# Performance work log

Hardware: AMD Instinct MI355X
Metric: run time of the kernel (lower is better)

Reference implementation:

```python
import jax, jax.numpy as jnp
import numpy as np

N_NODES = 100000
N_USERS = 60000
N_MOVIES = 40000
N_EDGES = 1200000
D_IN = 64
D_EMB = 64


def setup_inputs() -> dict:
    key = jax.random.key(0)
    ks = jax.random.split(key, 6)
    x = jax.random.normal(ks[0], (N_NODES, D_IN), dtype=jnp.float32)
    edge_index = jax.random.randint(ks[1], (2, N_EDGES), 0, N_NODES, dtype=jnp.int64)
    # Glorot-ish init for the two GCNConv linear weights
    W1 = jax.random.normal(ks[2], (D_IN, D_EMB), dtype=jnp.float32) * (1.0 / np.sqrt(D_IN))
    b1 = jnp.zeros((D_EMB,), dtype=jnp.float32)
    W2 = jax.random.normal(ks[3], (D_EMB, D_EMB), dtype=jnp.float32) * (1.0 / np.sqrt(D_EMB))
    b2 = jnp.zeros((D_EMB,), dtype=jnp.float32)
    return {"x": x, "edge_index": edge_index, "W1": W1, "b1": b1, "W2": W2, "b2": b2}


def gcn_conv(x, W, b, src, dst):
    """PyG GCNConv: D^{-1/2}(A+I)D^{-1/2} X W + b with symmetric norm and self-loops."""
    h = x @ W  # [N, D_out]
    ones = jnp.ones(src.shape[0], dtype=h.dtype)
    # degree includes self-loop (+1)
    deg = jax.ops.segment_sum(ones, dst, num_segments=N_NODES) + 1.0
    dinv = jax.lax.rsqrt(deg)  # [N]
    coef = dinv[src] * dinv[dst]  # [E]
    agg = jax.ops.segment_sum(h[src] * coef[:, None], dst, num_segments=N_NODES)
    # self-loop contribution: norm = dinv[i]^2
    return agg + h * (dinv * dinv)[:, None] + b


def reference(x, edge_index, W1, b1, W2, b2):
    src, dst = edge_index[0], edge_index[1]
    h = gcn_conv(x, W1, b1, src, dst)
    h = jax.nn.relu(h)  # dropout is identity in eval mode
    h = gcn_conv(h, W2, b2, src, dst)
    user = h[:N_USERS]
    movie = h[N_USERS:N_USERS + N_MOVIES]
    return user, movie, h
```

## Files before the change

kernel.cpp:

```cpp
#include <hip/hip_runtime.h>

#define NN 100000
#define NE 1200000
#define DD 64
#define NPART 8
#define PSZ (NN / NPART)
#define EPB 4096
#define NCHUNK ((NE + EPB - 1) / EPB)
#define SCH 1024
#define SNB ((NN + SCH - 1) / SCH)

#define KCH3 96
#define CEH3 (NE / KCH3)
#define P3 4
#define BINS3 (NN / P3)
#define BINW3 (BINS3 / 4)
#define KSEG 4
#define KPS (KCH3 / KSEG)
#define NW4 (NN / 4)

static __device__ __forceinline__ unsigned short f2bf(float f) {
    unsigned int u = __float_as_uint(f);
    u += 0x7fffu + ((u >> 16) & 1u);
    return (unsigned short)(u >> 16);
}
static __device__ __forceinline__ float bf_lo(unsigned int u) {
    return __uint_as_float(u << 16);
}
static __device__ __forceinline__ float bf_hi(unsigned int u) {
    return __uint_as_float(u & 0xffff0000u);
}

__global__ __launch_bounds__(1024) void k_hist3(const int* __restrict__ dst,
                                                unsigned char* __restrict__ H,
                                                unsigned char* __restrict__ rank8) {
    __shared__ unsigned int bins[BINW3];
    int k = blockIdx.x >> 2;
    int p = blockIdx.x & 3;
    int t = threadIdx.x;
    for (int i = t; i < BINW3; i += 1024) bins[i] = 0u;
    __syncthreads();
    int lo = p * BINS3;
    int beg = k * CEH3;
    for (int e4 = beg + t * 4; e4 < beg + CEH3; e4 += 4096) {
        int4 d4 = *(const int4*)&dst[e4];
        int dd[4] = {d4.x, d4.y, d4.z, d4.w};
#pragma unroll
        for (int j = 0; j < 4; ++j) {
            unsigned int r = (unsigned int)(dd[j] - lo);
            if (r < (unsigned int)BINS3) {
                unsigned int sh = (r & 3u) << 3;
                unsigned int old = atomicAdd(&bins[r >> 2], 1u << sh);
                rank8[e4 + j] = (unsigned char)((old >> sh) & 0xffu);
            }
        }
    }
    __syncthreads();
    unsigned int* Hw = (unsigned int*)(H + (size_t)k * NN + lo);
    for (int i = t; i < BINW3; i += 1024) Hw[i] = bins[i];
}

__global__ __launch_bounds__(256) void k_cseg_sum(const unsigned int* __restrict__ H32,
                                                  unsigned int* __restrict__ aux) {
    int wd = blockIdx.x * 256 + threadIdx.x;
    int seg = blockIdx.y;
    if (wd >= NW4) return;
    unsigned int s = 0;
#pragma unroll
    for (int k = 0; k < KPS; ++k)
        s += H32[(size_t)(seg * KPS + k) * NW4 + wd];
    aux[seg * NW4 + wd] = s;
}

__global__ __launch_bounds__(256) void k_cseg_scan(unsigned int* __restrict__ H32,
                                                   const unsigned int* __restrict__ aux,
                                                   int* __restrict__ degi) {
    int wd = blockIdx.x * 256 + threadIdx.x;
    int seg = blockIdx.y;
    if (wd >= NW4) return;
    unsigned int base = 0;
    for (int i = 0; i < seg; ++i) base += aux[i * NW4 + wd];
    unsigned int s = base;
#pragma unroll
    for (int k = 0; k < KPS; ++k) {
        size_t idx = (size_t)(seg * KPS + k) * NW4 + wd;
        unsigned int v = H32[idx];
        H32[idx] = s;
        s += v;
    }
    if (seg == KSEG - 1) {
        int4 dg;
        dg.x = (int)(s & 0xffu);
        dg.y = (int)((s >> 8) & 0xffu);
        dg.z = (int)((s >> 16) & 0xffu);
        dg.w = (int)(s >> 24);
        *(int4*)&degi[4 * wd] = dg;
    }
}

__global__ __launch_bounds__(256) void k_fill3(const int* __restrict__ src,
                                               const int* __restrict__ dst,
                                               const unsigned char* __restrict__ rank8,
                                               const unsigned char* __restrict__ H,
                                               const int* __restrict__ rowptr,
                                               int* __restrict__ csr) {
    int e4 = (blockIdx.x * 256 + threadIdx.x) * 4;
    if (e4 >= NE) return;
    int4 d4 = *(const int4*)&dst[e4];
    int4 s4 = *(const int4*)&src[e4];
    unsigned int r4 = *(const unsigned int*)&rank8[e4];
    int dd[4] = {d4.x, d4.y, d4.z, d4.w};
    int ss[4] = {s4.x, s4.y, s4.z, s4.w};
    int k = e4 / CEH3;
#pragma unroll
    for (int j = 0; j < 4; ++j) {
        int d = dd[j];
        int base = rowptr[d] + (int)H[(size_t)k * NN + d];
        csr[base + (int)((r4 >> (8 * j)) & 0xffu)] = ss[j];
    }
}

__global__ __launch_bounds__(256) void k_coef(const int* __restrict__ rowptr,
                                              const int* __restrict__ csr,
                                              const float* __restrict__ dinv,
                                              float* __restrict__ coef) {
    int n = blockIdx.x * 256 + threadIdx.x;
    if (n >= NN) return;
    int e = rowptr[n], end = rowptr[n + 1];
    float dn = dinv[n];
    for (; e < end; ++e) coef[e] = dinv[csr[e]] * dn;
}

__global__ void k_hist_rank(const int* __restrict__ dst, int* __restrict__ degi,
                            int* __restrict__ rank, int ne) {
    int i = blockIdx.x * blockDim.x + threadIdx.x;
    if (i < ne) rank[i] = atomicAdd(&degi[dst[i]], 1);
}

__global__ __launch_bounds__(256) void k_hist(const int* __restrict__ dst,
                                              int* __restrict__ degi, int ne) {
    int part = blockIdx.x & (NPART - 1);
    int lo = part * PSZ, hi = lo + PSZ;
    int beg = (blockIdx.x >> 3) * EPB;
    int end = min(beg + EPB, ne);
    for (int e = beg + (int)threadIdx.x; e < end; e += 256) {
        int d = dst[e];
        if (d >= lo && d < hi) atomicAdd(&degi[d], 1);
    }
}

__global__ __launch_bounds__(256) void k_scan_local(const int* __restrict__ degi,
                                                    int* __restrict__ rowptr,
                                                    int* __restrict__ part,
                                                    float* __restrict__ dinv) {
    __shared__ int wsum[4];
    int t = threadIdx.x;
    int idx = blockIdx.x * SCH + t * 4;
    int d0 = 0, d1 = 0, d2 = 0, d3 = 0;
    if (idx + 3 < NN) {
        int4 v = *(const int4*)&degi[idx];
        d0 = v.x; d1 = v.y; d2 = v.z; d3 = v.w;
        float4 dv;
        dv.x = rsqrtf((float)d0 + 1.0f);
        dv.y = rsqrtf((float)d1 + 1.0f);
        dv.z = rsqrtf((float)d2 + 1.0f);
        dv.w = rsqrtf((float)d3 + 1.0f);
        *(float4*)&dinv[idx] = dv;
    } else {
        if (idx     < NN) { d0 = degi[idx];     dinv[idx]     = rsqrtf((float)d0 + 1.0f); }
        if (idx + 1 < NN) { d1 = degi[idx + 1]; dinv[idx + 1] = rsqrtf((float)d1 + 1.0f); }
        if (idx + 2 < NN) { d2 = degi[idx + 2]; dinv[idx + 2] = rsqrtf((float)d2 + 1.0f); }
        if (idx + 3 < NN) { d3 = degi[idx + 3]; dinv[idx + 3] = rsqrtf((float)d3 + 1.0f); }
    }
    int s = d0 + d1 + d2 + d3;
    int lane = t & 63;
    int incl = s;
#pragma unroll
    for (int off = 1; off < 64; off <<= 1) {
        int v = __shfl_up(incl, off);
        if (lane >= off) incl += v;
    }
    int wv = t >> 6;
    if (lane == 63) wsum[wv] = incl;
    __syncthreads();
    int woff = 0;
#pragma unroll
    for (int i = 0; i < 4; ++i) if (i < wv) woff += wsum[i];
    int excl = woff + incl - s;
    if (idx     < NN) rowptr[idx]     = excl;
    if (idx + 1 < NN) rowptr[idx + 1] = excl + d0;
    if (idx + 2 < NN) rowptr[idx + 2] = excl + d0 + d1;
    if (idx + 3 < NN) rowptr[idx + 3] = excl + d0 + d1 + d2;
    if (t == 255) part[blockIdx.x] = woff + incl;
}

__global__ __launch_bounds__(128) void k_scan_part(int* __restrict__ part) {
    __shared__ int sm[128];
    int t = threadIdx.x;
    int v = (t < SNB) ? part[t] : 0;
    sm[t] = v;
    __syncthreads();
    for (int off = 1; off < 128; off <<= 1) {
        int add = (t >= off) ? sm[t - off] : 0;
        __syncthreads();
        sm[t] += add;
        __syncthreads();
    }
    if (t < SNB) part[t] = sm[t] - v;
}

__global__ void k_scan_add(int* __restrict__ rowptr, const int* __restrict__ part) {
    int i = blockIdx.x * blockDim.x + threadIdx.x;
    if (i < NN) rowptr[i] += part[i >> 10];
    if (i == 0) rowptr[NN] = NE;
}

__global__ void k_fill_rank(const int* __restrict__ src, const int* __restrict__ dst,
                            const int* __restrict__ rank, const int* __restrict__ rowptr,
                            int* __restrict__ csr_src, int ne) {
    int e = blockIdx.x * blockDim.x + threadIdx.x;
    if (e < ne) csr_src[rowptr[dst[e]] + rank[e]] = src[e];
}

__global__ __launch_bounds__(256) void k_fill(const int* __restrict__ src,
                                              const int* __restrict__ dst,
                                              const int* __restrict__ rowptr,
                                              int* __restrict__ cnt,
                                              int* __restrict__ csr_src, int ne) {
    int part = blockIdx.x & (NPART - 1);
    int lo = part * PSZ, hi = lo + PSZ;
    int beg = (blockIdx.x >> 3) * EPB;
    int end = min(beg + EPB, ne);
    for (int e = beg + (int)threadIdx.x; e < end; e += 256) {
        int d = dst[e];
        if (d >= lo && d < hi) {
            int pos = rowptr[d] + atomicAdd(&cnt[d], 1);
            csr_src[pos] = src[e];
        }
    }
}

__global__ __launch_bounds__(256) void k_gemm_bf(const float* __restrict__ X,
                                                 const float* __restrict__ W,
                                                 unsigned short* __restrict__ Hb,
                                                 int nrows) {
    __shared__ float4 Ws4[64][16];
    __shared__ float  Xs[64][68];
    int tid = threadIdx.x;
    const float4* W4 = (const float4*)W;
    for (int i = tid; i < 64 * 16; i += 256) Ws4[i >> 4][i & 15] = W4[i];
    int row0 = blockIdx.x * 64;
    const float4* X4 = (const float4*)X;
    for (int i = tid; i < 64 * 16; i += 256) {
        int r = i >> 4, q = i & 15;
        int row = row0 + r;
        float4 v = make_float4(0.f, 0.f, 0.f, 0.f);
        if (row < nrows) v = X4[row * 16 + q];
        *((float4*)&Xs[r][q * 4]) = v;
    }
    __syncthreads();
    int c4 = tid & 15;
    int rg = tid >> 4;
    float4 acc0 = make_float4(0.f, 0.f, 0.f, 0.f);
    float4 acc1 = acc0, acc2 = acc0, acc3 = acc0;
#pragma unroll 4
    for (int k = 0; k < 64; ++k) {
        float4 w = Ws4[k][c4];
        float x0 = Xs[rg * 4 + 0][k];
        float x1 = Xs[rg * 4 + 1][k];
        float x2 = Xs[rg * 4 + 2][k];
        float x3 = Xs[rg * 4 + 3][k];
        acc0.x += x0 * w.x; acc0.y += x0 * w.y; acc0.z += x0 * w.z; acc0.w += x0 * w.w;
        acc1.x += x1 * w.x; acc1.y += x1 * w.y; acc1.z += x1 * w.z; acc1.w += x1 * w.w;
        acc2.x += x2 * w.x; acc2.y += x2 * w.y; acc2.z += x2 * w.z; acc2.w += x2 * w.w;
        acc3.x += x3 * w.x; acc3.y += x3 * w.y; acc3.z += x3 * w.z; acc3.w += x3 * w.w;
    }
    float4 accs[4] = {acc0, acc1, acc2, acc3};
#pragma unroll
    for (int i = 0; i < 4; ++i) {
        int row = row0 + rg * 4 + i;
        if (row < nrows) {
            ushort4 o;
            o.x = f2bf(accs[i].x); o.y = f2bf(accs[i].y);
            o.z = f2bf(accs[i].z); o.w = f2bf(accs[i].w);
            *((ushort4*)&Hb[row * 64 + c4 * 4]) = o;
        }
    }
}

__global__ __launch_bounds__(256) void k_reduce(const unsigned short* __restrict__ Hb,
                                                const int* __restrict__ rowptr,
                                                const int* __restrict__ csr_src,
                                                const float* __restrict__ coef,
                                                const float* __restrict__ dinv,
                                                const float* __restrict__ b,
                                                float* __restrict__ out0,
                                                float* __restrict__ out1,
                                                int do_relu) {
    int n = blockIdx.x * 32 + (threadIdx.x >> 3);
    if (n >= NN) return;
    int cg = threadIdx.x & 7;
    float din = dinv[n];
    uint4 us = *(const uint4*)(Hb + (size_t)n * 64 + cg * 8);

    int e0 = rowptr[n];
    int deg = rowptr[n + 1] - e0;
    int dmax = deg;
    dmax = max(dmax, __shfl_xor(dmax, 8));
    dmax = max(dmax, __shfl_xor(dmax, 16));
    dmax = max(dmax, __shfl_xor(dmax, 32));

    float acc[8];
#pragma unroll
    for (int j = 0; j < 8; ++j) acc[j] = 0.f;

#define LDE(T, S, C) { bool _v = (T) < deg; \
                       S = _v ? csr_src[e0 + (T)] : 0; \
                       C = _v ? coef[e0 + (T)] : 0.f; }
#define GAT(U, S) U = *(const uint4*)(Hb + (size_t)(S) * 64 + cg * 8);
#define CONS(U, C) { acc[0] += bf_lo(U.x) * (C);  acc[1] += bf_hi(U.x) * (C); \
                     acc[2] += bf_lo(U.y) * (C);  acc[3] += bf_hi(U.y) * (C); \
                     acc[4] += bf_lo(U.z) * (C);  acc[5] += bf_hi(U.z) * (C); \
                     acc[6] += bf_lo(U.w) * (C);  acc[7] += bf_hi(U.w) * (C); }

    int s0, s1, s2, s3; float c0, c1, c2, c3;
    LDE(0, s0, c0); LDE(1, s1, c1); LDE(2, s2, c2); LDE(3, s3, c3);
    uint4 u0, u1, u2, u3;
    GAT(u0, s0); GAT(u1, s1); GAT(u2, s2); GAT(u3, s3);

    for (int t = 0; t < dmax; t += 4) {
        int sn0, sn1, sn2, sn3; float cn0, cn1, cn2, cn3;
        LDE(t + 4, sn0, cn0); LDE(t + 5, sn1, cn1);
        LDE(t + 6, sn2, cn2); LDE(t + 7, sn3, cn3);
        CONS(u0, c0); GAT(u0, sn0); c0 = cn0;
        CONS(u1, c1); GAT(u1, sn1); c1 = cn1;
        CONS(u2, c2); GAT(u2, sn2); c2 = cn2;
        CONS(u3, c3); GAT(u3, sn3); c3 = cn3;
    }
#undef LDE
#undef GAT
#undef CONS

    float dd = din * din;
    float4 b0 = *(const float4*)(b + cg * 8);
    float4 b1 = *(const float4*)(b + cg * 8 + 4);
    float4 o0, o1;
    o0.x = acc[0] + bf_lo(us.x) * dd + b0.x;
    o0.y = acc[1] + bf_hi(us.x) * dd + b0.y;
    o0.z = acc[2] + bf_lo(us.y) * dd + b0.z;
    o0.w = acc[3] + bf_hi(us.y) * dd + b0.w;
    o1.x = acc[4] + bf_lo(us.z) * dd + b1.x;
    o1.y = acc[5] + bf_hi(us.z) * dd + b1.y;
    o1.z = acc[6] + bf_lo(us.w) * dd + b1.z;
    o1.w = acc[7] + bf_hi(us.w) * dd + b1.w;
    if (do_relu) {
        o0.x = fmaxf(o0.x, 0.f); o0.y = fmaxf(o0.y, 0.f);
        o0.z = fmaxf(o0.z, 0.f); o0.w = fmaxf(o0.w, 0.f);
        o1.x = fmaxf(o1.x, 0.f); o1.y = fmaxf(o1.y, 0.f);
        o1.z = fmaxf(o1.z, 0.f); o1.w = fmaxf(o1.w, 0.f);
    }
    *(float4*)(out0 + (size_t)n * 64 + cg * 8)     = o0;
    *(float4*)(out0 + (size_t)n * 64 + cg * 8 + 4) = o1;
    if (out1) {
        *(float4*)(out1 + (size_t)n * 64 + cg * 8)     = o0;
        *(float4*)(out1 + (size_t)n * 64 + cg * 8 + 4) = o1;
    }
}

__global__ void k_copy4(const float4* __restrict__ in, float4* __restrict__ out, int n4) {
    int i = blockIdx.x * blockDim.x + threadIdx.x;
    if (i < n4) out[i] = in[i];
}

extern "C" void kernel_launch(void* const* d_in, const int* in_sizes, int n_in,
                              void* d_out, int out_size, void* d_ws, size_t ws_size,
                              hipStream_t stream) {
    const float* x  = (const float*)d_in[0];
    const int*   ei = (const int*)d_in[1];
    const float* W1 = (const float*)d_in[2];
    const float* b1 = (const float*)d_in[3];
    const float* W2 = (const float*)d_in[4];
    const float* b2 = (const float*)d_in[5];
    const int* src = ei;
    const int* dst = ei + NE;

    float* A = (float*)d_out;
    float* B = (float*)d_out + (size_t)NN * DD;

    char* w = (char*)d_ws;
    size_t off = 0;
    auto alloc = [&](size_t bytes) { void* p = w + off; off += (bytes + 255) & ~(size_t)255; return p; };
    float* dinv   = (float*)alloc(NN * sizeof(float));
    int*   degi   = (int*)  alloc(NN * sizeof(int));
    int*   cnt    = (int*)  alloc(NN * sizeof(int));
    int*   rowptr = (int*)  alloc((NN + 1) * sizeof(int));
    int*   part   = (int*)  alloc(512 * sizeof(int));
    int*   csr    = (int*)  alloc(NE * sizeof(int));
    float* coef   = (float*)alloc(NE * sizeof(float));
    size_t off_common = off;
    void* uni = alloc((size_t)NN * DD * sizeof(unsigned short));
    size_t off_uni = off;
    size_t need_rank = off_common + (((size_t)NE * sizeof(int) + 255) & ~(size_t)255);

    bool new_path  = (ws_size >= off_uni);
    bool rank_path = !new_path && (ws_size >= need_rank);

    unsigned char* Hh    = (unsigned char*)uni;
    unsigned char* rank8 = (unsigned char*)uni + (size_t)KCH3 * NN;
    int*           rank  = (int*)uni;
    unsigned short* Bb   = new_path ? (unsigned short*)uni : (unsigned short*)B;
    bool bb_in_ws = new_path;

    if (new_path) {
        k_hist3<<<KCH3 * P3, 1024, 0, stream>>>(dst, Hh, rank8);
        dim3 cgrid((NW4 + 255) / 256, KSEG);
        k_cseg_sum<<<cgrid, 256, 0, stream>>>((unsigned int*)Hh, (unsigned int*)cnt);
        k_cseg_scan<<<cgrid, 256, 0, stream>>>((unsigned int*)Hh, (const unsigned int*)cnt, degi);
        k_scan_local<<<SNB, 256, 0, stream>>>(degi, rowptr, part, dinv);
        k_scan_part<<<1, 128, 0, stream>>>(part);
        k_scan_add<<<(NN + 255) / 256, 256, 0, stream>>>(rowptr, part);
        k_fill3<<<(NE / 4 + 255) / 256, 256, 0, stream>>>(src, dst, rank8, Hh, rowptr, csr);
    } else if (rank_path) {
        hipMemsetAsync(degi, 0, NN * sizeof(int), stream);
        k_hist_rank<<<(NE + 255) / 256, 256, 0, stream>>>(dst, degi, rank, NE);
        k_scan_local<<<SNB, 256, 0, stream>>>(degi, rowptr, part, dinv);
        k_scan_part<<<1, 128, 0, stream>>>(part);
        k_scan_add<<<(NN + 255) / 256, 256, 0, stream>>>(rowptr, part);
        k_fill_rank<<<(NE + 255) / 256, 256, 0, stream>>>(src, dst, rank, rowptr, csr, NE);
    } else {
        hipMemsetAsync(degi, 0, NN * sizeof(int), stream);
        hipMemsetAsync(cnt, 0, NN * sizeof(int), stream);
        k_hist<<<NCHUNK * NPART, 256, 0, stream>>>(dst, degi, NE);
        k_scan_local<<<SNB, 256, 0, stream>>>(degi, rowptr, part, dinv);
        k_scan_part<<<1, 128, 0, stream>>>(part);
        k_scan_add<<<(NN + 255) / 256, 256, 0, stream>>>(rowptr, part);
        k_fill<<<NCHUNK * NPART, 256, 0, stream>>>(src, dst, rowptr, cnt, csr, NE);
    }
    k_coef<<<(NN + 255) / 256, 256, 0, stream>>>(rowptr, csr, dinv, coef);

    k_gemm_bf<<<(NN + 63) / 64, 256, 0, stream>>>(x, W1, Bb, NN);
    k_reduce<<<(NN + 31) / 32, 256, 0, stream>>>(Bb, rowptr, csr, coef, dinv, b1, A, nullptr, 1);

    k_gemm_bf<<<(NN + 63) / 64, 256, 0, stream>>>(A, W2, Bb, NN);
    if (bb_in_ws) {
        k_reduce<<<(NN + 31) / 32, 256, 0, stream>>>(Bb, rowptr, csr, coef, dinv, b2, A, B, 0);
    } else {
        k_reduce<<<(NN + 31) / 32, 256, 0, stream>>>(Bb, rowptr, csr, coef, dinv, b2, A, nullptr, 0);
        k_copy4<<<(NN * DD / 4 + 255) / 256, 256, 0, stream>>>((const float4*)A, (float4*)B, NN * DD / 4);
    }
}
```

Measured before the change: 250.2 us.

## Fuse histogram with layer-1 GEMM, fold scans, pack csr+coef, fuse reduce with GEMM2

```diff
diff --git a/kernel.cpp b/kernel.cpp
--- a/kernel.cpp
+++ b/kernel.cpp
@@ -18,46 +18,79 @@
 #define KSEG 4
 #define KPS (KCH3 / KSEG)
 #define NW4 (NN / 4)
+#define HISTB (KCH3 * P3)
+#define GEMMB ((NN + 255) / 256)
 
 static __device__ __forceinline__ unsigned short f2bf(float f) {
     unsigned int u = __float_as_uint(f);
     u += 0x7fffu + ((u >> 16) & 1u);
     return (unsigned short)(u >> 16);
 }
-static __device__ __forceinline__ float bf_lo(unsigned int u) {
-    return __uint_as_float(u << 16);
-}
-static __device__ __forceinline__ float bf_hi(unsigned int u) {
-    return __uint_as_float(u & 0xffff0000u);
-}
-
-__global__ __launch_bounds__(1024) void k_hist3(const int* __restrict__ dst,
-                                                unsigned char* __restrict__ H,
-                                                unsigned char* __restrict__ rank8) {
-    __shared__ unsigned int bins[BINW3];
-    int k = blockIdx.x >> 2;
-    int p = blockIdx.x & 3;
+static __device__ __forceinline__ float bf_lo(unsigned int u) { return __uint_as_float(u << 16); }
+static __device__ __forceinline__ float bf_hi(unsigned int u) { return __uint_as_float(u & 0xffff0000u); }
+
+__global__ __launch_bounds__(1024) void k_histgemm(const int* __restrict__ dst,
+                                                   unsigned char* __restrict__ H,
+                                                   unsigned char* __restrict__ rank8,
+                                                   const float* __restrict__ X,
+                                                   const float* __restrict__ W,
+                                                   unsigned short* __restrict__ Hb) {
+    __shared__ union SM {
+        unsigned int bins[BINW3];
+        struct { float4 Ws4[64][16]; float Xs[64][68]; } g;
+    } sm;
     int t = threadIdx.x;
-    for (int i = t; i < BINW3; i += 1024) bins[i] = 0u;
-    __syncthreads();
-    int lo = p * BINS3;
-    int beg = k * CEH3;
-    for (int e4 = beg + t * 4; e4 < beg + CEH3; e4 += 4096) {
-        int4 d4 = *(const int4*)&dst[e4];
-        int dd[4] = {d4.x, d4.y, d4.z, d4.w};
-#pragma unroll
-        for (int j = 0; j < 4; ++j) {
-            unsigned int r = (unsigned int)(dd[j] - lo);
-            if (r < (unsigned int)BINS3) {
-                unsigned int sh = (r & 3u) << 3;
-                unsigned int old = atomicAdd(&bins[r >> 2], 1u << sh);
-                rank8[e4 + j] = (unsigned char)((old >> sh) & 0xffu);
+    if (blockIdx.x < HISTB) {
+        int k = blockIdx.x >> 2;
+        int p = blockIdx.x & 3;
+        for (int i = t; i < BINW3; i += 1024) sm.bins[i] = 0u;
+        __syncthreads();
+        int lo = p * BINS3;
+        int beg = k * CEH3;
+        for (int e4 = beg + t * 4; e4 < beg + CEH3; e4 += 4096) {
+            int4 d4 = *(const int4*)&dst[e4];
+            int dd[4] = {d4.x, d4.y, d4.z, d4.w};
+#pragma unroll
+            for (int j = 0; j < 4; ++j) {
+                unsigned int r = (unsigned int)(dd[j] - lo);
+                if (r < (unsigned int)BINS3) {
+                    unsigned int sh = (r & 3u) << 3;
+                    unsigned int old = atomicAdd(&sm.bins[r >> 2], 1u << sh);
+                    rank8[e4 + j] = (unsigned char)((old >> sh) & 0xffu);
+                }
             }
         }
-    }
-    __syncthreads();
-    unsigned int* Hw = (unsigned int*)(H + (size_t)k * NN + lo);
-    for (int i = t; i < BINW3; i += 1024) Hw[i] = bins[i];
+        __syncthreads();
+        unsigned int* Hw = (unsigned int*)(H + (size_t)k * NN + lo);
+        for (int i = t; i < BINW3; i += 1024) Hw[i] = sm.bins[i];
+    } else {
+        const float4* W4 = (const float4*)W;
+        sm.g.Ws4[t >> 4][t & 15] = W4[t];
+        int row0 = (int)(blockIdx.x - HISTB) * 256;
+        const float4* X4 = (const float4*)X;
+        int r = t >> 4, q = t & 15;
+#pragma unroll
+        for (int s = 0; s < 4; ++s) {
+            int row = row0 + s * 64 + r;
+            float4 v = make_float4(0.f, 0.f, 0.f, 0.f);
+            if (row < NN) v = X4[row * 16 + q];
+            __syncthreads();
+            *((float4*)&sm.g.Xs[r][q * 4]) = v;
+            __syncthreads();
+            float4 acc = make_float4(0.f, 0.f, 0.f, 0.f);
+#pragma unroll 4
+            for (int k = 0; k < 64; ++k) {
+                float4 w = sm.g.Ws4[k][q];
+                float x = sm.g.Xs[r][k];
+                acc.x += x * w.x; acc.y += x * w.y; acc.z += x * w.z; acc.w += x * w.w;
+            }
+            if (row < NN) {
+                ushort4 o;
+                o.x = f2bf(acc.x); o.y = f2bf(acc.y); o.z = f2bf(acc.z); o.w = f2bf(acc.w);
+                *((ushort4*)&Hb[(size_t)row * 64 + q * 4]) = o;
+            }
+        }
+    }
 }
 
 __global__ __launch_bounds__(256) void k_cseg_sum(const unsigned int* __restrict__ H32,
@@ -72,38 +105,89 @@
     aux[seg * NW4 + wd] = s;
 }
 
-__global__ __launch_bounds__(256) void k_cseg_scan(unsigned int* __restrict__ H32,
-                                                   const unsigned int* __restrict__ aux,
-                                                   int* __restrict__ degi) {
-    int wd = blockIdx.x * 256 + threadIdx.x;
+__global__ __launch_bounds__(256) void k_cseg_scan2(unsigned int* __restrict__ H32,
+                                                    const unsigned int* __restrict__ aux,
+                                                    int* __restrict__ rowptr,
+                                                    int* __restrict__ part,
+                                                    float* __restrict__ dinv) {
+    __shared__ int wsum[4];
+    int t = threadIdx.x;
+    int wd = blockIdx.x * 256 + t;
     int seg = blockIdx.y;
-    if (wd >= NW4) return;
-    unsigned int base = 0;
-    for (int i = 0; i < seg; ++i) base += aux[i * NW4 + wd];
-    unsigned int s = base;
-#pragma unroll
-    for (int k = 0; k < KPS; ++k) {
-        size_t idx = (size_t)(seg * KPS + k) * NW4 + wd;
-        unsigned int v = H32[idx];
-        H32[idx] = s;
-        s += v;
-    }
-    if (seg == KSEG - 1) {
-        int4 dg;
-        dg.x = (int)(s & 0xffu);
-        dg.y = (int)((s >> 8) & 0xffu);
-        dg.z = (int)((s >> 16) & 0xffu);
-        dg.w = (int)(s >> 24);
-        *(int4*)&degi[4 * wd] = dg;
-    }
-}
-
-__global__ __launch_bounds__(256) void k_fill3(const int* __restrict__ src,
+    bool valid = wd < NW4;
+    unsigned int s = 0;
+    if (valid) {
+        unsigned int base = 0;
+        for (int i = 0; i < seg; ++i) base += aux[i * NW4 + wd];
+        s = base;
+#pragma unroll
+        for (int k = 0; k < KPS; ++k) {
+            size_t idx = (size_t)(seg * KPS + k) * NW4 + wd;
+            unsigned int v = H32[idx];
+            H32[idx] = s;
+            s += v;
+        }
+    }
+    if (seg != KSEG - 1) return;
+    int d0 = valid ? (int)(s & 0xffu) : 0;
+    int d1 = valid ? (int)((s >> 8) & 0xffu) : 0;
+    int d2 = valid ? (int)((s >> 16) & 0xffu) : 0;
+    int d3 = valid ? (int)(s >> 24) : 0;
+    int idx = blockIdx.x * SCH + t * 4;
+    if (valid) {
+        float4 dv;
+        dv.x = rsqrtf((float)d0 + 1.0f);
+        dv.y = rsqrtf((float)d1 + 1.0f);
+        dv.z = rsqrtf((float)d2 + 1.0f);
+        dv.w = rsqrtf((float)d3 + 1.0f);
+        *(float4*)&dinv[idx] = dv;
+    }
+    int ssum = d0 + d1 + d2 + d3;
+    int lane = t & 63;
+    int incl = ssum;
+#pragma unroll
+    for (int off = 1; off < 64; off <<= 1) {
+        int v = __shfl_up(incl, off);
+        if (lane >= off) incl += v;
+    }
+    int wv = t >> 6;
+    if (lane == 63) wsum[wv] = incl;
+    __syncthreads();
+    int woff = 0;
+#pragma unroll
+    for (int i = 0; i < 4; ++i) if (i < wv) woff += wsum[i];
+    int excl = woff + incl - ssum;
+    if (valid) {
+        int4 rp = make_int4(excl, excl + d0, excl + d0 + d1, excl + d0 + d1 + d2);
+        *(int4*)&rowptr[idx] = rp;
+    }
+    if (t == 255) part[blockIdx.x] = woff + incl;
+}
+
+__global__ __launch_bounds__(128) void k_scan_part(int* __restrict__ part, int* __restrict__ rowptr) {
+    __shared__ int sm[128];
+    int t = threadIdx.x;
+    int v = (t < SNB) ? part[t] : 0;
+    sm[t] = v;
+    __syncthreads();
+    for (int off = 1; off < 128; off <<= 1) {
+        int add = (t >= off) ? sm[t - off] : 0;
+        __syncthreads();
+        sm[t] += add;
+        __syncthreads();
+    }
+    if (t == SNB - 1) rowptr[NN] = v;
+    if (t < SNB) part[t] = sm[t] - v;
+}
+
+__global__ __launch_bounds__(256) void k_fill4(const int* __restrict__ src,
                                                const int* __restrict__ dst,
                                                const unsigned char* __restrict__ rank8,
                                                const unsigned char* __restrict__ H,
                                                const int* __restrict__ rowptr,
-                                               int* __restrict__ csr) {
+                                               const int* __restrict__ part,
+                                               const float* __restrict__ dinv,
+                                               int2* __restrict__ cc) {
     int e4 = (blockIdx.x * 256 + threadIdx.x) * 4;
     if (e4 >= NE) return;
     int4 d4 = *(const int4*)&dst[e4];
@@ -114,39 +198,17 @@
     int k = e4 / CEH3;
 #pragma unroll
     for (int j = 0; j < 4; ++j) {
-        int d = dd[j];
-        int base = rowptr[d] + (int)H[(size_t)k * NN + d];
-        csr[base + (int)((r4 >> (8 * j)) & 0xffu)] = ss[j];
-    }
-}
-
-__global__ __launch_bounds__(256) void k_coef(const int* __restrict__ rowptr,
-                                              const int* __restrict__ csr,
-                                              const float* __restrict__ dinv,
-                                              float* __restrict__ coef) {
-    int n = blockIdx.x * 256 + threadIdx.x;
-    if (n >= NN) return;
-    int e = rowptr[n], end = rowptr[n + 1];
-    float dn = dinv[n];
-    for (; e < end; ++e) coef[e] = dinv[csr[e]] * dn;
+        int d = dd[j], s = ss[j];
+        int base = rowptr[d] + part[d >> 10] + (int)H[(size_t)k * NN + d];
+        int pos = base + (int)((r4 >> (8 * j)) & 0xffu);
+        cc[pos] = make_int2(s, __float_as_int(dinv[s] * dinv[d]));
+    }
 }
 
 __global__ void k_hist_rank(const int* __restrict__ dst, int* __restrict__ degi,
                             int* __restrict__ rank, int ne) {
     int i = blockIdx.x * blockDim.x + threadIdx.x;
     if (i < ne) rank[i] = atomicAdd(&degi[dst[i]], 1);
-}
-
-__global__ __launch_bounds__(256) void k_hist(const int* __restrict__ dst,
-                                              int* __restrict__ degi, int ne) {
-    int part = blockIdx.x & (NPART - 1);
-    int lo = part * PSZ, hi = lo + PSZ;
-    int beg = (blockIdx.x >> 3) * EPB;
-    int end = min(beg + EPB, ne);
-    for (int e = beg + (int)threadIdx.x; e < end; e += 256) {
-        int d = dst[e];
-        if (d >= lo && d < hi) atomicAdd(&degi[d], 1);
-    }
 }
 
 __global__ __launch_bounds__(256) void k_scan_local(const int* __restrict__ degi,
@@ -194,21 +256,6 @@
     if (t == 255) part[blockIdx.x] = woff + incl;
 }
 
-__global__ __launch_bounds__(128) void k_scan_part(int* __restrict__ part) {
-    __shared__ int sm[128];
-    int t = threadIdx.x;
-    int v = (t < SNB) ? part[t] : 0;
-    sm[t] = v;
-    __syncthreads();
-    for (int off = 1; off < 128; off <<= 1) {
-        int add = (t >= off) ? sm[t - off] : 0;
-        __syncthreads();
-        sm[t] += add;
-        __syncthreads();
-    }
-    if (t < SNB) part[t] = sm[t] - v;
-}
-
 __global__ void k_scan_add(int* __restrict__ rowptr, const int* __restrict__ part) {
     int i = blockIdx.x * blockDim.x + threadIdx.x;
     if (i < NN) rowptr[i] += part[i >> 10];
@@ -222,21 +269,16 @@
     if (e < ne) csr_src[rowptr[dst[e]] + rank[e]] = src[e];
 }
 
-__global__ __launch_bounds__(256) void k_fill(const int* __restrict__ src,
-                                              const int* __restrict__ dst,
-                                              const int* __restrict__ rowptr,
-                                              int* __restrict__ cnt,
-                                              int* __restrict__ csr_src, int ne) {
-    int part = blockIdx.x & (NPART - 1);
-    int lo = part * PSZ, hi = lo + PSZ;
-    int beg = (blockIdx.x >> 3) * EPB;
-    int end = min(beg + EPB, ne);
-    for (int e = beg + (int)threadIdx.x; e < end; e += 256) {
-        int d = dst[e];
-        if (d >= lo && d < hi) {
-            int pos = rowptr[d] + atomicAdd(&cnt[d], 1);
-            csr_src[pos] = src[e];
-        }
+__global__ __launch_bounds__(256) void k_pack(const int* __restrict__ rowptr,
+                                              const int* __restrict__ csr,
+                                              const float* __restrict__ dinv,
+                                              int2* __restrict__ cc) {
+    int n = blockIdx.x * 256 + threadIdx.x;
+    if (n >= NN) return;
+    float dn = dinv[n];
+    for (int e = rowptr[n]; e < rowptr[n + 1]; ++e) {
+        int s = csr[e];
+        cc[e] = make_int2(s, __float_as_int(dinv[s] * dn));
     }
 }
 
@@ -288,46 +330,21 @@
     }
 }
 
-__global__ __launch_bounds__(256) void k_reduce(const unsigned short* __restrict__ Hb,
-                                                const int* __restrict__ rowptr,
-                                                const int* __restrict__ csr_src,
-                                                const float* __restrict__ coef,
-                                                const float* __restrict__ dinv,
-                                                const float* __restrict__ b,
-                                                float* __restrict__ out0,
-                                                float* __restrict__ out1,
-                                                int do_relu) {
-    int n = blockIdx.x * 32 + (threadIdx.x >> 3);
-    if (n >= NN) return;
-    int cg = threadIdx.x & 7;
-    float din = dinv[n];
-    uint4 us = *(const uint4*)(Hb + (size_t)n * 64 + cg * 8);
-
-    int e0 = rowptr[n];
-    int deg = rowptr[n + 1] - e0;
-    int dmax = deg;
-    dmax = max(dmax, __shfl_xor(dmax, 8));
-    dmax = max(dmax, __shfl_xor(dmax, 16));
-    dmax = max(dmax, __shfl_xor(dmax, 32));
-
-    float acc[8];
-#pragma unroll
-    for (int j = 0; j < 8; ++j) acc[j] = 0.f;
-
-#define LDE(T, S, C) { bool _v = (T) < deg; \
-                       S = _v ? csr_src[e0 + (T)] : 0; \
-                       C = _v ? coef[e0 + (T)] : 0.f; }
+static __device__ __forceinline__ void gather8(const unsigned short* __restrict__ Hb,
+                                               const int2* __restrict__ cc,
+                                               int e0, int deg, int dmax, int cg,
+                                               float acc[8]) {
+#define LDE(T, S, C) { bool _v = (T) < deg; int2 _w = _v ? cc[e0 + (T)] : make_int2(0, 0); \
+                       S = _w.x; C = __int_as_float(_w.y); }
 #define GAT(U, S) U = *(const uint4*)(Hb + (size_t)(S) * 64 + cg * 8);
 #define CONS(U, C) { acc[0] += bf_lo(U.x) * (C);  acc[1] += bf_hi(U.x) * (C); \
                      acc[2] += bf_lo(U.y) * (C);  acc[3] += bf_hi(U.y) * (C); \
                      acc[4] += bf_lo(U.z) * (C);  acc[5] += bf_hi(U.z) * (C); \
                      acc[6] += bf_lo(U.w) * (C);  acc[7] += bf_hi(U.w) * (C); }
-
     int s0, s1, s2, s3; float c0, c1, c2, c3;
     LDE(0, s0, c0); LDE(1, s1, c1); LDE(2, s2, c2); LDE(3, s3, c3);
     uint4 u0, u1, u2, u3;
     GAT(u0, s0); GAT(u1, s1); GAT(u2, s2); GAT(u3, s3);
-
     for (int t = 0; t < dmax; t += 4) {
         int sn0, sn1, sn2, sn3; float cn0, cn1, cn2, cn3;
         LDE(t + 4, sn0, cn0); LDE(t + 5, sn1, cn1);
@@ -340,36 +357,123 @@
 #undef LDE
 #undef GAT
 #undef CONS
-
-    float dd = din * din;
-    float4 b0 = *(const float4*)(b + cg * 8);
-    float4 b1 = *(const float4*)(b + cg * 8 + 4);
+}
+
+__global__ __launch_bounds__(256) void k_reduce_g2(const unsigned short* __restrict__ Hb,
+                                                   const int* __restrict__ rowptr,
+                                                   const int* __restrict__ part,
+                                                   const int2* __restrict__ cc,
+                                                   const float* __restrict__ dinv,
+                                                   const float* __restrict__ bias,
+                                                   const float* __restrict__ W2,
+                                                   unsigned short* __restrict__ Hb2) {
+    __shared__ float4 Ws4[64][16];
+    __shared__ float rows[32][68];
+    int t = threadIdx.x;
+    const float4* W4 = (const float4*)W2;
+    for (int i = t; i < 1024; i += 256) Ws4[i >> 4][i & 15] = W4[i];
+
+    int n = blockIdx.x * 32 + (t >> 3);
+    int cg = t & 7;
+    bool nv = n < NN;
+    float din = nv ? dinv[n] : 0.f;
+    uint4 us = make_uint4(0u, 0u, 0u, 0u);
+    int e0 = 0, deg = 0;
+    if (nv) {
+        us = *(const uint4*)(Hb + (size_t)n * 64 + cg * 8);
+        int rp0 = rowptr[n] + part[n >> 10];
+        int rp1 = rowptr[n + 1] + part[(n + 1) >> 10];
+        e0 = rp0; deg = rp1 - rp0;
+    }
+    int dmax = deg;
+    dmax = max(dmax, __shfl_xor(dmax, 8));
+    dmax = max(dmax, __shfl_xor(dmax, 16));
+    dmax = max(dmax, __shfl_xor(dmax, 32));
+
+    float acc[8];
+#pragma unroll
+    for (int j = 0; j < 8; ++j) acc[j] = 0.f;
+    gather8(Hb, cc, e0, deg, dmax, cg, acc);
+
+    float ddn = din * din;
+    float4 b0 = *(const float4*)(bias + cg * 8);
+    float4 b1 = *(const float4*)(bias + cg * 8 + 4);
     float4 o0, o1;
-    o0.x = acc[0] + bf_lo(us.x) * dd + b0.x;
-    o0.y = acc[1] + bf_hi(us.x) * dd + b0.y;
-    o0.z = acc[2] + bf_lo(us.y) * dd + b0.z;
-    o0.w = acc[3] + bf_hi(us.y) * dd + b0.w;
-    o1.x = acc[4] + bf_lo(us.z) * dd + b1.x;
-    o1.y = acc[5] + bf_hi(us.z) * dd + b1.y;
-    o1.z = acc[6] + bf_lo(us.w) * dd + b1.z;
-    o1.w = acc[7] + bf_hi(us.w) * dd + b1.w;
-    if (do_relu) {
-        o0.x = fmaxf(o0.x, 0.f); o0.y = fmaxf(o0.y, 0.f);
-        o0.z = fmaxf(o0.z, 0.f); o0.w = fmaxf(o0.w, 0.f);
-        o1.x = fmaxf(o1.x, 0.f); o1.y = fmaxf(o1.y, 0.f);
-        o1.z = fmaxf(o1.z, 0.f); o1.w = fmaxf(o1.w, 0.f);
-    }
+    o0.x = fmaxf(acc[0] + bf_lo(us.x) * ddn + b0.x, 0.f);
+    o0.y = fmaxf(acc[1] + bf_hi(us.x) * ddn + b0.y, 0.f);
+    o0.z = fmaxf(acc[2] + bf_lo(us.y) * ddn + b0.z, 0.f);
+    o0.w = fmaxf(acc[3] + bf_hi(us.y) * ddn + b0.w, 0.f);
+    o1.x = fmaxf(acc[4] + bf_lo(us.z) * ddn + b1.x, 0.f);
+    o1.y = fmaxf(acc[5] + bf_hi(us.z) * ddn + b1.y, 0.f);
+    o1.z = fmaxf(acc[6] + bf_lo(us.w) * ddn + b1.z, 0.f);
+    o1.w = fmaxf(acc[7] + bf_hi(us.w) * ddn + b1.w, 0.f);
+    int node = t >> 3;
+    *(float4*)&rows[node][cg * 8]     = o0;
+    *(float4*)&rows[node][cg * 8 + 4] = o1;
+    __syncthreads();
+
+    int c2 = t & 7;
+    float a0 = 0.f, a1 = 0.f, a2 = 0.f, a3 = 0.f, a4 = 0.f, a5 = 0.f, a6 = 0.f, a7 = 0.f;
+#pragma unroll 4
+    for (int k = 0; k < 64; ++k) {
+        float r = rows[node][k];
+        float4 w0 = Ws4[k][c2 * 2];
+        float4 w1 = Ws4[k][c2 * 2 + 1];
+        a0 += r * w0.x; a1 += r * w0.y; a2 += r * w0.z; a3 += r * w0.w;
+        a4 += r * w1.x; a5 += r * w1.y; a6 += r * w1.z; a7 += r * w1.w;
+    }
+    if (nv) {
+        uint4 pk;
+        pk.x = (unsigned int)f2bf(a0) | ((unsigned int)f2bf(a1) << 16);
+        pk.y = (unsigned int)f2bf(a2) | ((unsigned int)f2bf(a3) << 16);
+        pk.z = (unsigned int)f2bf(a4) | ((unsigned int)f2bf(a5) << 16);
+        pk.w = (unsigned int)f2bf(a6) | ((unsigned int)f2bf(a7) << 16);
+        *(uint4*)&Hb2[(size_t)n * 64 + c2 * 8] = pk;
+    }
+}
+
+__global__ __launch_bounds__(256) void k_reduce2(const unsigned short* __restrict__ Hb,
+                                                 const int* __restrict__ rowptr,
+                                                 const int* __restrict__ part,
+                                                 const int2* __restrict__ cc,
+                                                 const float* __restrict__ dinv,
+                                                 const float* __restrict__ bias,
+                                                 float* __restrict__ out0,
+                                                 float* __restrict__ out1) {
+    int n = blockIdx.x * 32 + (threadIdx.x >> 3);
+    if (n >= NN) return;
+    int cg = threadIdx.x & 7;
+    float din = dinv[n];
+    uint4 us = *(const uint4*)(Hb + (size_t)n * 64 + cg * 8);
+    int rp0 = rowptr[n] + part[n >> 10];
+    int rp1 = rowptr[n + 1] + part[(n + 1) >> 10];
+    int e0 = rp0, deg = rp1 - rp0;
+    int dmax = deg;
+    dmax = max(dmax, __shfl_xor(dmax, 8));
+    dmax = max(dmax, __shfl_xor(dmax, 16));
+    dmax = max(dmax, __shfl_xor(dmax, 32));
+
+    float acc[8];
+#pragma unroll
+    for (int j = 0; j < 8; ++j) acc[j] = 0.f;
+    gather8(Hb, cc, e0, deg, dmax, cg, acc);
+
+    float ddn = din * din;
+    float4 b0 = *(const float4*)(bias + cg * 8);
+    float4 b1 = *(const float4*)(bias + cg * 8 + 4);
+    float4 o0, o1;
+    o0.x = acc[0] + bf_lo(us.x) * ddn + b0.x;
+    o0.y = acc[1] + bf_hi(us.x) * ddn + b0.y;
+    o0.z = acc[2] + bf_lo(us.y) * ddn + b0.z;
+    o0.w = acc[3] + bf_hi(us.y) * ddn + b0.w;
+    o1.x = acc[4] + bf_lo(us.z) * ddn + b1.x;
+    o1.y = acc[5] + bf_hi(us.z) * ddn + b1.y;
+    o1.z = acc[6] + bf_lo(us.w) * ddn + b1.z;
+    o1.w = acc[7] + bf_hi(us.w) * ddn + b1.w;
     *(float4*)(out0 + (size_t)n * 64 + cg * 8)     = o0;
     *(float4*)(out0 + (size_t)n * 64 + cg * 8 + 4) = o1;
-    if (out1) {
-        *(float4*)(out1 + (size_t)n * 64 + cg * 8)     = o0;
-        *(float4*)(out1 + (size_t)n * 64 + cg * 8 + 4) = o1;
-    }
-}
-
-__global__ void k_copy4(const float4* __restrict__ in, float4* __restrict__ out, int n4) {
-    int i = blockIdx.x * blockDim.x + threadIdx.x;
-    if (i < n4) out[i] = in[i];
+    *(float4*)(out1 + (size_t)n * 64 + cg * 8)     = o0;
+    *(float4*)(out1 + (size_t)n * 64 + cg * 8 + 4) = o1;
 }
 
 extern "C" void kernel_launch(void* const* d_in, const int* in_sizes, int n_in,
@@ -396,56 +500,38 @@
     int*   rowptr = (int*)  alloc((NN + 1) * sizeof(int));
     int*   part   = (int*)  alloc(512 * sizeof(int));
     int*   csr    = (int*)  alloc(NE * sizeof(int));
-    float* coef   = (float*)alloc(NE * sizeof(float));
-    size_t off_common = off;
-    void* uni = alloc((size_t)NN * DD * sizeof(unsigned short));
-    size_t off_uni = off;
-    size_t need_rank = off_common + (((size_t)NE * sizeof(int) + 255) & ~(size_t)255);
-
-    bool new_path  = (ws_size >= off_uni);
-    bool rank_path = !new_path && (ws_size >= need_rank);
-
+    int2*  cc     = (int2*) alloc(NE * sizeof(int2));
+    void*  uni    = alloc((size_t)NN * DD * sizeof(unsigned short));
     unsigned char* Hh    = (unsigned char*)uni;
     unsigned char* rank8 = (unsigned char*)uni + (size_t)KCH3 * NN;
-    int*           rank  = (int*)uni;
-    unsigned short* Bb   = new_path ? (unsigned short*)uni : (unsigned short*)B;
-    bool bb_in_ws = new_path;
+    unsigned short* Bb2  = (unsigned short*)uni;
+    unsigned short* Bb1 = (unsigned short*)alloc((size_t)NN * DD * sizeof(unsigned short));
+    int* rank = (int*)Bb1;
+    size_t off_total = off;
+
+    bool new_path = (ws_size >= off_total);
 
     if (new_path) {
-        k_hist3<<<KCH3 * P3, 1024, 0, stream>>>(dst, Hh, rank8);
+        k_histgemm<<<HISTB + GEMMB, 1024, 0, stream>>>(dst, Hh, rank8, x, W1, Bb1);
         dim3 cgrid((NW4 + 255) / 256, KSEG);
         k_cseg_sum<<<cgrid, 256, 0, stream>>>((unsigned int*)Hh, (unsigned int*)cnt);
-        k_cseg_scan<<<cgrid, 256, 0, stream>>>((unsigned int*)Hh, (const unsigned int*)cnt, degi);
-        k_scan_local<<<SNB, 256, 0, stream>>>(degi, rowptr, part, dinv);
-        k_scan_part<<<1, 128, 0, stream>>>(part);
-        k_scan_add<<<(NN + 255) / 256, 256, 0, stream>>>(rowptr, part);
-        k_fill3<<<(NE / 4 + 255) / 256, 256, 0, stream>>>(src, dst, rank8, Hh, rowptr, csr);
-    } else if (rank_path) {
+        k_cseg_scan2<<<cgrid, 256, 0, stream>>>((unsigned int*)Hh, (const unsigned int*)cnt,
+                                                rowptr, part, dinv);
+        k_scan_part<<<1, 128, 0, stream>>>(part, rowptr);
+        k_fill4<<<(NE / 4 + 255) / 256, 256, 0, stream>>>(src, dst, rank8, Hh, rowptr, part, dinv, cc);
+        k_reduce_g2<<<(NN + 31) / 32, 256, 0, stream>>>(Bb1, rowptr, part, cc, dinv, b1, W2, Bb2);
+        k_reduce2<<<(NN + 31) / 32, 256, 0, stream>>>(Bb2, rowptr, part, cc, dinv, b2, A, B);
+    } else {
         hipMemsetAsync(degi, 0, NN * sizeof(int), stream);
         k_hist_rank<<<(NE + 255) / 256, 256, 0, stream>>>(dst, degi, rank, NE);
         k_scan_local<<<SNB, 256, 0, stream>>>(degi, rowptr, part, dinv);
-        k_scan_part<<<1, 128, 0, stream>>>(part);
+        k_scan_part<<<1, 128, 0, stream>>>(part, rowptr);
         k_scan_add<<<(NN + 255) / 256, 256, 0, stream>>>(rowptr, part);
+        hipMemsetAsync(part, 0, 512 * sizeof(int), stream);
         k_fill_rank<<<(NE + 255) / 256, 256, 0, stream>>>(src, dst, rank, rowptr, csr, NE);
-    } else {
-        hipMemsetAsync(degi, 0, NN * sizeof(int), stream);
-        hipMemsetAsync(cnt, 0, NN * sizeof(int), stream);
-        k_hist<<<NCHUNK * NPART, 256, 0, stream>>>(dst, degi, NE);
-        k_scan_local<<<SNB, 256, 0, stream>>>(degi, rowptr, part, dinv);
-        k_scan_part<<<1, 128, 0, stream>>>(part);
-        k_scan_add<<<(NN + 255) / 256, 256, 0, stream>>>(rowptr, part);
-        k_fill<<<NCHUNK * NPART, 256, 0, stream>>>(src, dst, rowptr, cnt, csr, NE);
-    }
-    k_coef<<<(NN + 255) / 256, 256, 0, stream>>>(rowptr, csr, dinv, coef);
-
-    k_gemm_bf<<<(NN + 63) / 64, 256, 0, stream>>>(x, W1, Bb, NN);
-    k_reduce<<<(NN + 31) / 32, 256, 0, stream>>>(Bb, rowptr, csr, coef, dinv, b1, A, nullptr, 1);
-
-    k_gemm_bf<<<(NN + 63) / 64, 256, 0, stream>>>(A, W2, Bb, NN);
-    if (bb_in_ws) {
-        k_reduce<<<(NN + 31) / 32, 256, 0, stream>>>(Bb, rowptr, csr, coef, dinv, b2, A, B, 0);
-    } else {
-        k_reduce<<<(NN + 31) / 32, 256, 0, stream>>>(Bb, rowptr, csr, coef, dinv, b2, A, nullptr, 0);
-        k_copy4<<<(NN * DD / 4 + 255) / 256, 256, 0, stream>>>((const float4*)A, (float4*)B, NN * DD / 4);
-    }
-}
+        k_pack<<<(NN + 255) / 256, 256, 0, stream>>>(rowptr, csr, dinv, cc);
+        k_gemm_bf<<<(NN + 63) / 64, 256, 0, stream>>>(x, W1, Bb1, NN);
+        k_reduce_g2<<<(NN + 31) / 32, 256, 0, stream>>>(Bb1, rowptr, part, cc, dinv, b1, W2, Bb2);
+        k_reduce2<<<(NN + 31) / 32, 256, 0, stream>>>(Bb2, rowptr, part, cc, dinv, b2, A, B);
+    }
+}
```

Result: faster. 233.9 us (-6.5%).
